# Performance work log

Measured on AMD Instinct MI355X. Metric: run time of the kernel, lower is better.

The kernel has to match this reference:

```python
import jax, jax.numpy as jnp
import numpy as np

B, T, F, H = 256, 4096, 16, 64

def setup_inputs() -> dict:
    key = jax.random.key(0)
    ks = jax.random.split(key, 16)
    rn = lambda k, s, sc=0.1: jax.random.normal(k, s, dtype=jnp.float32) * sc
    return {
        'x':    rn(ks[0], (B, T, F), 1.0),
        'Wi1':  rn(ks[1], (F, 3 * H)), 'bi1': jnp.zeros((3 * H,), jnp.float32),
        'Whr1': rn(ks[2], (H, H)), 'Whz1': rn(ks[3], (H, H)), 'Whn1': rn(ks[4], (H, H)),
        'bhn1': jnp.zeros((H,), jnp.float32),
        'Wi2':  rn(ks[5], (H, 3 * H)), 'bi2': jnp.zeros((3 * H,), jnp.float32),
        'Whr2': rn(ks[6], (H, H)), 'Whz2': rn(ks[7], (H, H)), 'Whn2': rn(ks[8], (H, H)),
        'bhn2': jnp.zeros((H,), jnp.float32),
        'Wp':   rn(ks[9], (F, H)), 'bp': jnp.zeros((H,), jnp.float32),
        'Wa':   rn(ks[10], (H, 1)), 'ba': jnp.zeros((1,), jnp.float32),
        'W1':   rn(ks[11], (H, 128)), 'b1': jnp.zeros((128,), jnp.float32),
        'W2':   rn(ks[12], (128, 64)), 'b2': jnp.zeros((64,), jnp.float32),
        'W3':   rn(ks[13], (64, 32)), 'b3': jnp.zeros((32,), jnp.float32),
        'W4':   rn(ks[14], (32, 2)), 'b4': jnp.zeros((2,), jnp.float32),
    }

def gru_layer(x, Wi, bi, Whr, Whz, Whn, bhn):
    # flax GRUCell math: r/z hidden kernels bias-free; n hidden kernel has bias.
    b, h = x.shape[0], Whr.shape[0]
    xi = jnp.einsum('btf,fk->btk', x, Wi) + bi  # precompute input projections (B,T,3H)
    def step(hprev, xt):
        ir, iz, inn = jnp.split(xt, 3, axis=-1)
        r = jax.nn.sigmoid(ir + hprev @ Whr)
        z = jax.nn.sigmoid(iz + hprev @ Whz)
        n = jnp.tanh(inn + r * (hprev @ Whn + bhn))
        hnew = (1.0 - z) * n + z * hprev
        return hnew, hnew
    h0 = jnp.zeros((b, h), x.dtype)
    _, ys = jax.lax.scan(step, h0, jnp.swapaxes(xi, 0, 1))  # (T,B,H)
    return jnp.swapaxes(ys, 0, 1)  # (B,T,H)

def reference(x, Wi1, bi1, Whr1, Whz1, Whn1, bhn1,
              Wi2, bi2, Whr2, Whz2, Whn2, bhn2,
              Wp, bp, Wa, ba, W1, b1, W2, b2, W3, b3, W4, b4):
    o1 = gru_layer(x, Wi1, bi1, Whr1, Whz1, Whn1, bhn1)
    x_proj = jnp.einsum('btf,fh->bth', x, Wp) + bp  # F != H -> project
    o1 = o1 + 0.5 * x_proj
    o2 = gru_layer(o1, Wi2, bi2, Whr2, Whz2, Whn2, bhn2) + 0.5 * o1
    scores = jnp.einsum('bth,ho->bto', o2, Wa) + ba  # (B,T,1)
    w = jax.nn.softmax(scores, axis=1)
    attended = jnp.sum(o2 * w, axis=1)  # (B,H)
    h1 = jax.nn.relu(attended @ W1 + b1)
    h2 = jax.nn.relu(h1 @ W2 + b2)
    h3 = jax.nn.relu(h2 @ W3 + b3)
    return h3 @ W4 + b4  # (B,2)
```

## Files before the change

kernel.cpp:

```cpp
#include <hip/hip_runtime.h>


#define B_ 256
#define T_ 4096
#define F_ 16
#define H_ 64
#define L2E 1.4426950408889634f

typedef float v2f __attribute__((ext_vector_type(2)));

__device__ __forceinline__ float rdlane(float v, int lane) {
    return __builtin_bit_cast(float, __builtin_amdgcn_readlane(__builtin_bit_cast(int, v), lane));
}
__device__ __forceinline__ float sigm(float x) {
    float e = __builtin_amdgcn_exp2f(-L2E * x);
    return __builtin_amdgcn_rcpf(1.0f + e);
}
__device__ __forceinline__ float tanh_(float x) {
    float e = __builtin_amdgcn_exp2f(2.0f * L2E * x);
    return 1.0f - 2.0f * __builtin_amdgcn_rcpf(1.0f + e);
}
__device__ __forceinline__ v2f fma2(v2f a, v2f b, v2f c) {
    return __builtin_elementwise_fma(a, b, c);
}

#define DPPADD(x, ctrl) \
    ((x) + __builtin_bit_cast(float, __builtin_amdgcn_update_dpp( \
        0, __builtin_bit_cast(int, (x)), (ctrl), 0xF, 0xF, true)))

__device__ __forceinline__ float qsum(float x) {
    float s = DPPADD(x, 0xB1);
    return DPPADD(s, 0x4E);
}
__device__ __forceinline__ float wred(float x) {
    x = DPPADD(x, 0x111);
    x = DPPADD(x, 0x112);
    x = DPPADD(x, 0x114);
    x = DPPADD(x, 0x118);
    x = DPPADD(x, 0x142);
    x = DPPADD(x, 0x143);
    return x;
}

__launch_bounds__(256, 1)
__global__ void solar_rnn(const float* __restrict__ x,
                          const float* __restrict__ Wi1, const float* __restrict__ bi1,
                          const float* __restrict__ Whr1, const float* __restrict__ Whz1,
                          const float* __restrict__ Whn1, const float* __restrict__ bhn1,
                          const float* __restrict__ Wi2, const float* __restrict__ bi2,
                          const float* __restrict__ Whr2, const float* __restrict__ Whz2,
                          const float* __restrict__ Whn2, const float* __restrict__ bhn2,
                          const float* __restrict__ Wp, const float* __restrict__ bp,
                          const float* __restrict__ Wa,
                          const float* __restrict__ W1, const float* __restrict__ b1,
                          const float* __restrict__ W2, const float* __restrict__ b2,
                          const float* __restrict__ W3, const float* __restrict__ b3,
                          const float* __restrict__ W4, const float* __restrict__ b4,
                          float* __restrict__ out)
{
    const int b   = blockIdx.x;
    const int tid = threadIdx.x;
    const int v   = tid >> 6;
    const int j   = tid & 63;
    const int oj  = 16 * v + (j >> 2);

    __shared__ __align__(16) float red[2][5][256][2];
    __shared__ float sp[2][64];
    __shared__ float sm_a[128];
    __shared__ float sm_b[128];

    const int wslot = (v + (j >> 3)) & 3;
    const int widx  = 4 * j + wslot;
    const int ridx  = 64 * v + j;

    v2f wr1p[8], wz1p[8], wn1p[8];
    v2f wr2p[8], wz2p[8], wn2p[8];
    v2f u2rp[8], u2zp[8], u2np[8];
    #pragma unroll
    for (int m = 0; m < 8; ++m) {
        const int r0 = 16 * v + 2 * m, r1 = r0 + 1;
        wr1p[m] = v2f{Whr1[r0 * H_ + j], Whr1[r1 * H_ + j]};
        wz1p[m] = v2f{Whz1[r0 * H_ + j], Whz1[r1 * H_ + j]};
        wn1p[m] = v2f{Whn1[r0 * H_ + j], Whn1[r1 * H_ + j]};
        wr2p[m] = v2f{Whr2[r0 * H_ + j], Whr2[r1 * H_ + j]};
        wz2p[m] = v2f{Whz2[r0 * H_ + j], Whz2[r1 * H_ + j]};
        wn2p[m] = v2f{Whn2[r0 * H_ + j], Whn2[r1 * H_ + j]};
        u2rp[m] = v2f{Wi2[r0 * 192 + j],       Wi2[r1 * 192 + j]};
        u2zp[m] = v2f{Wi2[r0 * 192 + 64 + j],  Wi2[r1 * 192 + 64 + j]};
        u2np[m] = v2f{Wi2[r0 * 192 + 128 + j], Wi2[r1 * 192 + 128 + j]};
    }
    float x2r[4], x2z[4], x2n[4];
    #pragma unroll
    for (int kk = 0; kk < 4; ++kk) {
        const int row = 4 * v + kk;
        float ar = 0.f, az = 0.f, an = 0.f;
        for (int m = 0; m < H_; ++m) {
            const float wp = Wp[row * H_ + m];
            ar = fmaf(wp, Wi2[m * 192 + j],       ar);
            az = fmaf(wp, Wi2[m * 192 + 64 + j],  az);
            an = fmaf(wp, Wi2[m * 192 + 128 + j], an);
        }
        x2r[kk] = 0.5f * ar; x2z[kk] = 0.5f * az; x2n[kk] = 0.5f * an;
    }
    v2f w1rp[2], w1zp[2], w1np[2], wpvp[2], x2rp[2], x2zp[2], x2np[2];
    #pragma unroll
    for (int m = 0; m < 2; ++m) {
        const int r0 = 4 * v + 2 * m, r1 = r0 + 1;
        w1rp[m] = v2f{Wi1[r0 * 192 + j],       Wi1[r1 * 192 + j]};
        w1zp[m] = v2f{Wi1[r0 * 192 + 64 + j],  Wi1[r1 * 192 + 64 + j]};
        w1np[m] = v2f{Wi1[r0 * 192 + 128 + j], Wi1[r1 * 192 + 128 + j]};
        wpvp[m] = v2f{Wp[r0 * H_ + j],         Wp[r1 * H_ + j]};
        x2rp[m] = v2f{x2r[2 * m], x2r[2 * m + 1]};
        x2zp[m] = v2f{x2z[2 * m], x2z[2 * m + 1]};
        x2np[m] = v2f{x2n[2 * m], x2n[2 * m + 1]};
    }
    float cbr = 0.f, cbz = 0.f, cbn = 0.f;
    for (int m = 0; m < H_; ++m) {
        const float bpm = bp[m];
        cbr = fmaf(bpm, Wi2[m * 192 + oj],       cbr);
        cbz = fmaf(bpm, Wi2[m * 192 + 64 + oj],  cbz);
        cbn = fmaf(bpm, Wi2[m * 192 + 128 + oj], cbn);
    }
    const float b1r = bi1[oj], b1z = bi1[64 + oj], b1n = bi1[128 + oj], bh1o = bhn1[oj];
    const float bb2r = bi2[oj]       + 0.5f * cbr;
    const float bb2z = bi2[64 + oj]  + 0.5f * cbz;
    const float bb2n = bi2[128 + oj] + 0.5f * cbn;
    const float bh2o = bhn2[oj];
    const float bpo  = bp[oj], wao = Wa[oj];

    float h1 = 0.f, h2 = 0.f, o1p = 0.f, o2a = 0.f;
    float am = -3.0e38f, al = 0.f, aa = 0.f;
    v2f sH1p[8], sH2p[8];
    #pragma unroll
    for (int m = 0; m < 8; ++m) { sH1p[m] = v2f{0.f, 0.f}; sH2p[m] = v2f{0.f, 0.f}; }

    const float* xb = x + (size_t)b * T_ * F_;
    float4 xq_cur  = *(const float4*)(xb + ((size_t)j * F_ + 4 * v));
    float4 xq_next = *(const float4*)(xb + ((size_t)(64 + j) * F_ + 4 * v));

    v2f cxp0, cxp1;

    {
        const float a0 = rdlane(xq_cur.x, 0), a1 = rdlane(xq_cur.y, 0),
                    a2 = rdlane(xq_cur.z, 0), a3 = rdlane(xq_cur.w, 0);
        const v2f ap0 = v2f{a0, a1}, ap1 = v2f{a2, a3};
        const v2f zz = v2f{0.f, 0.f};
        v2f arp = fma2(w1rp[0], ap0, fma2(w1rp[1], ap1, zz));
        v2f azp = fma2(w1zp[0], ap0, fma2(w1zp[1], ap1, zz));
        v2f anp = fma2(w1np[0], ap0, fma2(w1np[1], ap1, zz));
        v2f axp = fma2(wpvp[0], ap0, fma2(wpvp[1], ap1, zz));
        *(v2f*)&red[0][0][widx][0] = v2f{arp.x + arp.y, azp.x + azp.y};
        *(v2f*)&red[0][1][widx][0] = v2f{anp.x + anp.y, 0.f};
        *(v2f*)&red[0][2][widx][0] = v2f{axp.x + axp.y, 0.f};
        cxp0 = ap0; cxp1 = ap1;
    }
    __syncthreads();

    {
        const v2f q0 = *(const v2f*)&red[0][0][ridx][0];
        const v2f q1 = *(const v2f*)&red[0][1][ridx][0];
        const v2f q2 = *(const v2f*)&red[0][2][ridx][0];
        const float g0 = qsum(q0.x), g1 = qsum(q0.y);
        const float g2 = qsum(q1.x), g3 = qsum(q1.y);
        const float g4 = qsum(q2.x);
        const float r1 = sigm(g0 + b1r);
        const float z1 = sigm(g1 + b1z);
        const float n1 = tanh_((g2 + b1n) + r1 * (g3 + bh1o));
        h1 = n1 + z1 * (h1 - n1);
        o1p = h1 + 0.5f * (g4 + bpo);
        #pragma unroll
        for (int m = 0; m < 8; ++m)
            sH1p[m] = v2f{rdlane(h1, 8 * m), rdlane(h1, 8 * m + 4)};

        const float xn0 = rdlane(xq_cur.x, 1), xn1 = rdlane(xq_cur.y, 1),
                    xn2 = rdlane(xq_cur.z, 1), xn3 = rdlane(xq_cur.w, 1);
        const v2f xp0 = v2f{xn0, xn1}, xp1 = v2f{xn2, xn3};
        const v2f zz = v2f{0.f, 0.f};

        v2f Aar2 = fma2(x2rp[0], cxp0, fma2(x2rp[1], cxp1, zz));
        v2f Aaz2 = fma2(x2zp[0], cxp0, fma2(x2zp[1], cxp1, zz));
        v2f Aan2 = fma2(x2np[0], cxp0, fma2(x2np[1], cxp1, zz));
        #pragma unroll
        for (int m = 0; m < 8; ++m) {
            Aar2 = fma2(sH1p[m], u2rp[m], Aar2);
            Aaz2 = fma2(sH1p[m], u2zp[m], Aaz2);
            Aan2 = fma2(sH1p[m], u2np[m], Aan2);
        }
        v2f Aar1 = fma2(w1rp[0], xp0, fma2(w1rp[1], xp1, zz));
        v2f Aaz1 = fma2(w1zp[0], xp0, fma2(w1zp[1], xp1, zz));
        v2f Aan1 = fma2(w1np[0], xp0, fma2(w1np[1], xp1, zz));
        v2f Aax1 = fma2(wpvp[0], xp0, fma2(wpvp[1], xp1, zz));
        v2f Ahn1 = zz;
        #pragma unroll
        for (int m = 0; m < 8; ++m) {
            Aar1 = fma2(sH1p[m], wr1p[m], Aar1);
            Aaz1 = fma2(sH1p[m], wz1p[m], Aaz1);
            Ahn1 = fma2(sH1p[m], wn1p[m], Ahn1);
        }
        *(v2f*)&red[1][0][widx][0] = v2f{Aar1.x + Aar1.y, Aaz1.x + Aaz1.y};
        *(v2f*)&red[1][1][widx][0] = v2f{Aan1.x + Aan1.y, Ahn1.x + Ahn1.y};
        *(v2f*)&red[1][2][widx][0] = v2f{Aax1.x + Aax1.y, Aan2.x + Aan2.y};
        *(v2f*)&red[1][3][widx][0] = v2f{Aar2.x + Aar2.y, Aaz2.x + Aaz2.y};
        *(v2f*)&red[1][4][widx][0] = v2f{0.f, 0.f};
        cxp0 = xp0; cxp1 = xp1;
    }
    __syncthreads();

    #pragma unroll 1
    for (int t = 1; t < T_; ++t) {
        const int pb = t & 1, qb = pb ^ 1;
        const int u = t + 1;
        if ((u & 63) == 0) {
            xq_cur = xq_next;
            const int c = (u >> 6) + 1;
            if (c < T_ / 64)
                xq_next = *(const float4*)(xb + (size_t)(c * 64 + j) * F_ + 4 * v);
        }
        const int ul = u & 63;
        const v2f xp0 = v2f{rdlane(xq_cur.x, ul), rdlane(xq_cur.y, ul)};
        const v2f xp1 = v2f{rdlane(xq_cur.z, ul), rdlane(xq_cur.w, ul)};

        const v2f q0 = *(const v2f*)&red[pb][0][ridx][0];
        const v2f q1 = *(const v2f*)&red[pb][1][ridx][0];
        const v2f q2 = *(const v2f*)&red[pb][2][ridx][0];
        const v2f q3 = *(const v2f*)&red[pb][3][ridx][0];
        const v2f q4 = *(const v2f*)&red[pb][4][ridx][0];
        float gp = sp[pb][j & 3];

        const v2f zz = v2f{0.f, 0.f};
        v2f Aar1 = fma2(w1rp[0], xp0, fma2(w1rp[1], xp1, zz));
        v2f Aaz1 = fma2(w1zp[0], xp0, fma2(w1zp[1], xp1, zz));
        v2f Aan1 = fma2(w1np[0], xp0, fma2(w1np[1], xp1, zz));
        v2f Aax1 = fma2(wpvp[0], xp0, fma2(wpvp[1], xp1, zz));
        v2f Aar2 = fma2(x2rp[0], cxp0, fma2(x2rp[1], cxp1, zz));
        v2f Aaz2 = fma2(x2zp[0], cxp0, fma2(x2zp[1], cxp1, zz));
        v2f Aan2 = fma2(x2np[0], cxp0, fma2(x2np[1], cxp1, zz));
        v2f Ahn1 = zz, Ahn2 = zz;

        const float g0 = qsum(q0.x), g1 = qsum(q0.y);
        const float g2 = qsum(q1.x), g3 = qsum(q1.y);
        const float g4 = qsum(q2.x), g5 = qsum(q2.y);
        const float g6 = qsum(q3.x), g7 = qsum(q3.y);
        const float g8 = qsum(q4.x);
        gp = qsum(gp);

        if (t >= 2) {
            const float p  = 0.25f * gp;
            const float mn = fmaxf(am, p);
            const float ca = __builtin_amdgcn_exp2f((am - mn) * L2E);
            const float ce = __builtin_amdgcn_exp2f((p  - mn) * L2E);
            al = fmaf(al, ca, ce);
            aa = fmaf(aa, ca, ce * o2a);
            am = mn;
        }

        const float r2 = sigm(g6 + bb2r);
        const float z2 = sigm(g7 + bb2z);
        const float n2 = tanh_((g5 + bb2n) + r2 * (g8 + bh2o));
        h2 = n2 + z2 * (h2 - n2);
        const float o2 = h2 + 0.5f * o1p;
        float ps = wred(o2 * wao);
        if (j == 63) sp[qb][v] = ps;
        o2a = o2;
        #pragma unroll
        for (int m = 0; m < 8; ++m)
            sH2p[m] = v2f{rdlane(h2, 8 * m), rdlane(h2, 8 * m + 4)};

        const float r1 = sigm(g0 + b1r);
        const float z1 = sigm(g1 + b1z);
        const float n1 = tanh_((g2 + b1n) + r1 * (g3 + bh1o));
        h1 = n1 + z1 * (h1 - n1);
        o1p = h1 + 0.5f * (g4 + bpo);
        #pragma unroll
        for (int m = 0; m < 8; ++m)
            sH1p[m] = v2f{rdlane(h1, 8 * m), rdlane(h1, 8 * m + 4)};

        #pragma unroll
        for (int m = 0; m < 8; ++m) {
            Aar2 = fma2(sH2p[m], wr2p[m], Aar2);
            Aaz2 = fma2(sH2p[m], wz2p[m], Aaz2);
            Ahn2 = fma2(sH2p[m], wn2p[m], Ahn2);
        }
        #pragma unroll
        for (int m = 0; m < 8; ++m) {
            Aar2 = fma2(sH1p[m], u2rp[m], Aar2);
            Aaz2 = fma2(sH1p[m], u2zp[m], Aaz2);
            Aan2 = fma2(sH1p[m], u2np[m], Aan2);
        }
        #pragma unroll
        for (int m = 0; m < 8; ++m) {
            Aar1 = fma2(sH1p[m], wr1p[m], Aar1);
            Aaz1 = fma2(sH1p[m], wz1p[m], Aaz1);
            Ahn1 = fma2(sH1p[m], wn1p[m], Ahn1);
        }

        *(v2f*)&red[qb][0][widx][0] = v2f{Aar1.x + Aar1.y, Aaz1.x + Aaz1.y};
        *(v2f*)&red[qb][1][widx][0] = v2f{Aan1.x + Aan1.y, Ahn1.x + Ahn1.y};
        *(v2f*)&red[qb][2][widx][0] = v2f{Aax1.x + Aax1.y, Aan2.x + Aan2.y};
        *(v2f*)&red[qb][3][widx][0] = v2f{Aar2.x + Aar2.y, Aaz2.x + Aaz2.y};
        *(v2f*)&red[qb][4][widx][0] = v2f{Ahn2.x + Ahn2.y, 0.f};

        cxp0 = xp0; cxp1 = xp1;
        __syncthreads();
    }

    {
        const v2f q2 = *(const v2f*)&red[0][2][ridx][0];
        const v2f q3 = *(const v2f*)&red[0][3][ridx][0];
        const v2f q4 = *(const v2f*)&red[0][4][ridx][0];
        const float g5 = qsum(q2.y);
        const float g6 = qsum(q3.x), g7 = qsum(q3.y);
        const float g8 = qsum(q4.x);
        float gp = qsum(sp[0][j & 3]);
        {
            const float p  = 0.25f * gp;
            const float mn = fmaxf(am, p);
            const float ca = __builtin_amdgcn_exp2f((am - mn) * L2E);
            const float ce = __builtin_amdgcn_exp2f((p  - mn) * L2E);
            al = fmaf(al, ca, ce);
            aa = fmaf(aa, ca, ce * o2a);
            am = mn;
        }
        const float r2 = sigm(g6 + bb2r);
        const float z2 = sigm(g7 + bb2z);
        const float n2 = tanh_((g5 + bb2n) + r2 * (g8 + bh2o));
        h2 = n2 + z2 * (h2 - n2);
        const float o2 = h2 + 0.5f * o1p;
        float ps = wred(o2 * wao);
        if (j == 63) sp[1][v] = ps;
        __syncthreads();
        float gq = qsum(sp[1][j & 3]);
        {
            const float p  = 0.25f * gq;
            const float mn = fmaxf(am, p);
            const float ca = __builtin_amdgcn_exp2f((am - mn) * L2E);
            const float ce = __builtin_amdgcn_exp2f((p  - mn) * L2E);
            al = fmaf(al, ca, ce);
            aa = fmaf(aa, ca, ce * o2);
            am = mn;
        }
    }

    if ((j & 3) == 0) sm_a[oj] = aa / al;
    __syncthreads();

    float v1 = 0.f;
    if (tid < 128) {
        float a = b1[tid];
        for (int k = 0; k < 64; ++k) a = fmaf(sm_a[k], W1[k * 128 + tid], a);
        v1 = fmaxf(a, 0.f);
    }
    __syncthreads();
    if (tid < 128) sm_b[tid] = v1;
    __syncthreads();
    if (tid < 64) {
        float a = b2[tid];
        for (int k = 0; k < 128; ++k) a = fmaf(sm_b[k], W2[k * 64 + tid], a);
        sm_a[tid] = fmaxf(a, 0.f);
    }
    __syncthreads();
    if (tid < 32) {
        float a = b3[tid];
        for (int k = 0; k < 64; ++k) a = fmaf(sm_a[k], W3[k * 32 + tid], a);
        sm_b[tid] = fmaxf(a, 0.f);
    }
    __syncthreads();
    if (tid < 2) {
        float a = b4[tid];
        for (int k = 0; k < 32; ++k) a = fmaf(sm_b[k], W4[k * 2 + tid], a);
        out[b * 2 + tid] = a;
    }
}

extern "C" void kernel_launch(void* const* d_in, const int* in_sizes, int n_in,
                              void* d_out, int out_size, void* d_ws, size_t ws_size,
                              hipStream_t stream) {
    const float* x    = (const float*)d_in[0];
    const float* Wi1  = (const float*)d_in[1];
    const float* bi1  = (const float*)d_in[2];
    const float* Whr1 = (const float*)d_in[3];
    const float* Whz1 = (const float*)d_in[4];
    const float* Whn1 = (const float*)d_in[5];
    const float* bhn1 = (const float*)d_in[6];
    const float* Wi2  = (const float*)d_in[7];
    const float* bi2  = (const float*)d_in[8];
    const float* Whr2 = (const float*)d_in[9];
    const float* Whz2 = (const float*)d_in[10];
    const float* Whn2 = (const float*)d_in[11];
    const float* bhn2 = (const float*)d_in[12];
    const float* Wp   = (const float*)d_in[13];
    const float* bp   = (const float*)d_in[14];
    const float* Wa   = (const float*)d_in[15];
    const float* W1   = (const float*)d_in[17];
    const float* b1   = (const float*)d_in[18];
    const float* W2   = (const float*)d_in[19];
    const float* b2   = (const float*)d_in[20];
    const float* W3   = (const float*)d_in[21];
    const float* b3   = (const float*)d_in[22];
    const float* W4   = (const float*)d_in[23];
    const float* b4   = (const float*)d_in[24];

    solar_rnn<<<dim3(B_), dim3(256), 0, stream>>>(
        x, Wi1, bi1, Whr1, Whz1, Whn1, bhn1,
        Wi2, bi2, Whr2, Whz2, Whn2, bhn2,
        Wp, bp, Wa, W1, b1, W2, b2, W3, b3, W4, b4,
        (float*)d_out);
}
```

Before: 3.010 ms.

## Reorganize GRU recurrence so each quad owns an output column, exchanging hidden state via LDS

The recurrence is restructured so that each group of 4 lanes computes the full dot product for one output column, splitting the K dimension across the quad, and finishes with a quad DPP sum. Before, each wave handled a K-slice, hidden-state values were broadcast with readlane, and partial sums went through LDS. Now only the new h1/h2 vectors are written to double-buffered shared memory and read back as float4, which removes the 5-slot partial-sum exchange and the 16 readlanes per step. x is staged through a double-buffered LDS tile refilled every 16 steps, and the pipeline prologue is folded into the loop with a t==0 guard. The cost is more LDS reads per step and possible bank conflicts on the h vectors.

```diff
diff --git a/kernel.cpp b/kernel.cpp
--- a/kernel.cpp
+++ b/kernel.cpp
@@ -9,9 +9,6 @@
 
 typedef float v2f __attribute__((ext_vector_type(2)));
 
-__device__ __forceinline__ float rdlane(float v, int lane) {
-    return __builtin_bit_cast(float, __builtin_amdgcn_readlane(__builtin_bit_cast(int, v), lane));
-}
 __device__ __forceinline__ float sigm(float x) {
     float e = __builtin_amdgcn_exp2f(-L2E * x);
     return __builtin_amdgcn_rcpf(1.0f + e);
@@ -29,8 +26,8 @@
         0, __builtin_bit_cast(int, (x)), (ctrl), 0xF, 0xF, true)))
 
 __device__ __forceinline__ float qsum(float x) {
-    float s = DPPADD(x, 0xB1);
-    return DPPADD(s, 0x4E);
+    float t = DPPADD(x, 0xB1);
+    return DPPADD(t, 0x4E);
 }
 __device__ __forceinline__ float wred(float x) {
     x = DPPADD(x, 0x111);
@@ -62,54 +59,63 @@
     const int tid = threadIdx.x;
     const int v   = tid >> 6;
     const int j   = tid & 63;
-    const int oj  = 16 * v + (j >> 2);
-
-    __shared__ __align__(16) float red[2][5][256][2];
-    __shared__ float sp[2][64];
+    const int o   = j >> 2;
+    const int s   = j & 3;
+    const int col = 16 * v + o;
+
+    __shared__ __align__(16) float h1p[2][H_];
+    __shared__ __align__(16) float h2p[2][H_];
+    __shared__ __align__(16) float xbuf[2][256];
+    __shared__ float spl[2][4];
     __shared__ float sm_a[128];
     __shared__ float sm_b[128];
 
-    const int wslot = (v + (j >> 3)) & 3;
-    const int widx  = 4 * j + wslot;
-    const int ridx  = 64 * v + j;
+    int hoff[4];
+    #pragma unroll
+    for (int q = 0; q < 4; ++q) hoff[q] = 16 * s + 4 * ((q + s) & 3);
 
     v2f wr1p[8], wz1p[8], wn1p[8];
     v2f wr2p[8], wz2p[8], wn2p[8];
     v2f u2rp[8], u2zp[8], u2np[8];
     #pragma unroll
-    for (int m = 0; m < 8; ++m) {
-        const int r0 = 16 * v + 2 * m, r1 = r0 + 1;
-        wr1p[m] = v2f{Whr1[r0 * H_ + j], Whr1[r1 * H_ + j]};
-        wz1p[m] = v2f{Whz1[r0 * H_ + j], Whz1[r1 * H_ + j]};
-        wn1p[m] = v2f{Whn1[r0 * H_ + j], Whn1[r1 * H_ + j]};
-        wr2p[m] = v2f{Whr2[r0 * H_ + j], Whr2[r1 * H_ + j]};
-        wz2p[m] = v2f{Whz2[r0 * H_ + j], Whz2[r1 * H_ + j]};
-        wn2p[m] = v2f{Whn2[r0 * H_ + j], Whn2[r1 * H_ + j]};
-        u2rp[m] = v2f{Wi2[r0 * 192 + j],       Wi2[r1 * 192 + j]};
-        u2zp[m] = v2f{Wi2[r0 * 192 + 64 + j],  Wi2[r1 * 192 + 64 + j]};
-        u2np[m] = v2f{Wi2[r0 * 192 + 128 + j], Wi2[r1 * 192 + 128 + j]};
+    for (int q = 0; q < 4; ++q) {
+        const int rb = hoff[q];
+        #pragma unroll
+        for (int e = 0; e < 2; ++e) {
+            const int r0 = rb + 2 * e, r1 = r0 + 1;
+            const int m = 2 * q + e;
+            wr1p[m] = v2f{Whr1[r0 * H_ + col], Whr1[r1 * H_ + col]};
+            wz1p[m] = v2f{Whz1[r0 * H_ + col], Whz1[r1 * H_ + col]};
+            wn1p[m] = v2f{Whn1[r0 * H_ + col], Whn1[r1 * H_ + col]};
+            wr2p[m] = v2f{Whr2[r0 * H_ + col], Whr2[r1 * H_ + col]};
+            wz2p[m] = v2f{Whz2[r0 * H_ + col], Whz2[r1 * H_ + col]};
+            wn2p[m] = v2f{Whn2[r0 * H_ + col], Whn2[r1 * H_ + col]};
+            u2rp[m] = v2f{Wi2[r0 * 192 + col],       Wi2[r1 * 192 + col]};
+            u2zp[m] = v2f{Wi2[r0 * 192 + 64 + col],  Wi2[r1 * 192 + 64 + col]};
+            u2np[m] = v2f{Wi2[r0 * 192 + 128 + col], Wi2[r1 * 192 + 128 + col]};
+        }
     }
     float x2r[4], x2z[4], x2n[4];
     #pragma unroll
     for (int kk = 0; kk < 4; ++kk) {
-        const int row = 4 * v + kk;
+        const int row = 4 * s + kk;
         float ar = 0.f, az = 0.f, an = 0.f;
         for (int m = 0; m < H_; ++m) {
             const float wp = Wp[row * H_ + m];
-            ar = fmaf(wp, Wi2[m * 192 + j],       ar);
-            az = fmaf(wp, Wi2[m * 192 + 64 + j],  az);
-            an = fmaf(wp, Wi2[m * 192 + 128 + j], an);
+            ar = fmaf(wp, Wi2[m * 192 + col],       ar);
+            az = fmaf(wp, Wi2[m * 192 + 64 + col],  az);
+            an = fmaf(wp, Wi2[m * 192 + 128 + col], an);
         }
         x2r[kk] = 0.5f * ar; x2z[kk] = 0.5f * az; x2n[kk] = 0.5f * an;
     }
     v2f w1rp[2], w1zp[2], w1np[2], wpvp[2], x2rp[2], x2zp[2], x2np[2];
     #pragma unroll
     for (int m = 0; m < 2; ++m) {
-        const int r0 = 4 * v + 2 * m, r1 = r0 + 1;
-        w1rp[m] = v2f{Wi1[r0 * 192 + j],       Wi1[r1 * 192 + j]};
-        w1zp[m] = v2f{Wi1[r0 * 192 + 64 + j],  Wi1[r1 * 192 + 64 + j]};
-        w1np[m] = v2f{Wi1[r0 * 192 + 128 + j], Wi1[r1 * 192 + 128 + j]};
-        wpvp[m] = v2f{Wp[r0 * H_ + j],         Wp[r1 * H_ + j]};
+        const int r0 = 4 * s + 2 * m, r1 = r0 + 1;
+        w1rp[m] = v2f{Wi1[r0 * 192 + col],       Wi1[r1 * 192 + col]};
+        w1zp[m] = v2f{Wi1[r0 * 192 + 64 + col],  Wi1[r1 * 192 + 64 + col]};
+        w1np[m] = v2f{Wi1[r0 * 192 + 128 + col], Wi1[r1 * 192 + 128 + col]};
+        wpvp[m] = v2f{Wp[r0 * H_ + col],         Wp[r1 * H_ + col]};
         x2rp[m] = v2f{x2r[2 * m], x2r[2 * m + 1]};
         x2zp[m] = v2f{x2z[2 * m], x2z[2 * m + 1]};
         x2np[m] = v2f{x2n[2 * m], x2n[2 * m + 1]};
@@ -117,131 +123,82 @@
     float cbr = 0.f, cbz = 0.f, cbn = 0.f;
     for (int m = 0; m < H_; ++m) {
         const float bpm = bp[m];
-        cbr = fmaf(bpm, Wi2[m * 192 + oj],       cbr);
-        cbz = fmaf(bpm, Wi2[m * 192 + 64 + oj],  cbz);
-        cbn = fmaf(bpm, Wi2[m * 192 + 128 + oj], cbn);
-    }
-    const float b1r = bi1[oj], b1z = bi1[64 + oj], b1n = bi1[128 + oj], bh1o = bhn1[oj];
-    const float bb2r = bi2[oj]       + 0.5f * cbr;
-    const float bb2z = bi2[64 + oj]  + 0.5f * cbz;
-    const float bb2n = bi2[128 + oj] + 0.5f * cbn;
-    const float bh2o = bhn2[oj];
-    const float bpo  = bp[oj], wao = Wa[oj];
+        cbr = fmaf(bpm, Wi2[m * 192 + col],       cbr);
+        cbz = fmaf(bpm, Wi2[m * 192 + 64 + col],  cbz);
+        cbn = fmaf(bpm, Wi2[m * 192 + 128 + col], cbn);
+    }
+    const float b1r = bi1[col], b1z = bi1[64 + col], b1n = bi1[128 + col], bh1o = bhn1[col];
+    const float bb2r = bi2[col]       + 0.5f * cbr;
+    const float bb2z = bi2[64 + col]  + 0.5f * cbz;
+    const float bb2n = bi2[128 + col] + 0.5f * cbn;
+    const float bh2o = bhn2[col];
+    const float bpo  = bp[col], wao = Wa[col];
+
+    if (tid < 64) { h1p[0][j] = 0.f; h1p[1][j] = 0.f; h2p[0][j] = 0.f; h2p[1][j] = 0.f; }
+    if (tid < 8)  spl[tid >> 2][tid & 3] = 0.f;
+    const float* xb = x + (size_t)b * T_ * F_;
+    float4 xnext;
+    if (tid < 64) {
+        const float4* gx = (const float4*)xb;
+        ((float4*)xbuf[0])[j] = gx[j];
+        xnext = gx[64 + j];
+    }
+    __syncthreads();
 
     float h1 = 0.f, h2 = 0.f, o1p = 0.f, o2a = 0.f;
     float am = -3.0e38f, al = 0.f, aa = 0.f;
-    v2f sH1p[8], sH2p[8];
-    #pragma unroll
-    for (int m = 0; m < 8; ++m) { sH1p[m] = v2f{0.f, 0.f}; sH2p[m] = v2f{0.f, 0.f}; }
-
-    const float* xb = x + (size_t)b * T_ * F_;
-    float4 xq_cur  = *(const float4*)(xb + ((size_t)j * F_ + 4 * v));
-    float4 xq_next = *(const float4*)(xb + ((size_t)(64 + j) * F_ + 4 * v));
-
-    v2f cxp0, cxp1;
-
-    {
-        const float a0 = rdlane(xq_cur.x, 0), a1 = rdlane(xq_cur.y, 0),
-                    a2 = rdlane(xq_cur.z, 0), a3 = rdlane(xq_cur.w, 0);
-        const v2f ap0 = v2f{a0, a1}, ap1 = v2f{a2, a3};
+    v2f xprev0 = v2f{0.f, 0.f}, xprev1 = v2f{0.f, 0.f};
+
+    #pragma unroll 1
+    for (int t = 0; t < T_; ++t) {
+        const int tb = t & 1;
+
+        const float4 xt4 = ((const float4*)xbuf[(t >> 4) & 1])[(t & 15) * 4 + s];
+        const float* h1r = h1p[tb ^ 1];
+        const float* h2r = h2p[tb];
+        v2f hv1[8], hv2[8];
+        #pragma unroll
+        for (int q = 0; q < 4; ++q) {
+            const float4 a = *(const float4*)&h1r[hoff[q]];
+            const float4 c = *(const float4*)&h2r[hoff[q]];
+            hv1[2 * q]     = v2f{a.x, a.y};
+            hv1[2 * q + 1] = v2f{a.z, a.w};
+            hv2[2 * q]     = v2f{c.x, c.y};
+            hv2[2 * q + 1] = v2f{c.z, c.w};
+        }
+        float gp = spl[tb][s];
+
         const v2f zz = v2f{0.f, 0.f};
-        v2f arp = fma2(w1rp[0], ap0, fma2(w1rp[1], ap1, zz));
-        v2f azp = fma2(w1zp[0], ap0, fma2(w1zp[1], ap1, zz));
-        v2f anp = fma2(w1np[0], ap0, fma2(w1np[1], ap1, zz));
-        v2f axp = fma2(wpvp[0], ap0, fma2(wpvp[1], ap1, zz));
-        *(v2f*)&red[0][0][widx][0] = v2f{arp.x + arp.y, azp.x + azp.y};
-        *(v2f*)&red[0][1][widx][0] = v2f{anp.x + anp.y, 0.f};
-        *(v2f*)&red[0][2][widx][0] = v2f{axp.x + axp.y, 0.f};
-        cxp0 = ap0; cxp1 = ap1;
-    }
-    __syncthreads();
-
-    {
-        const v2f q0 = *(const v2f*)&red[0][0][ridx][0];
-        const v2f q1 = *(const v2f*)&red[0][1][ridx][0];
-        const v2f q2 = *(const v2f*)&red[0][2][ridx][0];
-        const float g0 = qsum(q0.x), g1 = qsum(q0.y);
-        const float g2 = qsum(q1.x), g3 = qsum(q1.y);
-        const float g4 = qsum(q2.x);
-        const float r1 = sigm(g0 + b1r);
-        const float z1 = sigm(g1 + b1z);
-        const float n1 = tanh_((g2 + b1n) + r1 * (g3 + bh1o));
-        h1 = n1 + z1 * (h1 - n1);
-        o1p = h1 + 0.5f * (g4 + bpo);
-        #pragma unroll
-        for (int m = 0; m < 8; ++m)
-            sH1p[m] = v2f{rdlane(h1, 8 * m), rdlane(h1, 8 * m + 4)};
-
-        const float xn0 = rdlane(xq_cur.x, 1), xn1 = rdlane(xq_cur.y, 1),
-                    xn2 = rdlane(xq_cur.z, 1), xn3 = rdlane(xq_cur.w, 1);
-        const v2f xp0 = v2f{xn0, xn1}, xp1 = v2f{xn2, xn3};
-        const v2f zz = v2f{0.f, 0.f};
-
-        v2f Aar2 = fma2(x2rp[0], cxp0, fma2(x2rp[1], cxp1, zz));
-        v2f Aaz2 = fma2(x2zp[0], cxp0, fma2(x2zp[1], cxp1, zz));
-        v2f Aan2 = fma2(x2np[0], cxp0, fma2(x2np[1], cxp1, zz));
+        v2f Aar2 = fma2(x2rp[0], xprev0, fma2(x2rp[1], xprev1, zz));
+        v2f Aaz2 = fma2(x2zp[0], xprev0, fma2(x2zp[1], xprev1, zz));
+        v2f Aan2 = fma2(x2np[0], xprev0, fma2(x2np[1], xprev1, zz));
+        const v2f xt0 = v2f{xt4.x, xt4.y}, xt1 = v2f{xt4.z, xt4.w};
+        v2f Aar1 = fma2(w1rp[0], xt0, fma2(w1rp[1], xt1, zz));
+        v2f Aaz1 = fma2(w1zp[0], xt0, fma2(w1zp[1], xt1, zz));
+        v2f Aan1 = fma2(w1np[0], xt0, fma2(w1np[1], xt1, zz));
+        v2f Aax1 = fma2(wpvp[0], xt0, fma2(wpvp[1], xt1, zz));
+        v2f Ahn1 = zz, Ahn2 = zz;
         #pragma unroll
         for (int m = 0; m < 8; ++m) {
-            Aar2 = fma2(sH1p[m], u2rp[m], Aar2);
-            Aaz2 = fma2(sH1p[m], u2zp[m], Aaz2);
-            Aan2 = fma2(sH1p[m], u2np[m], Aan2);
-        }
-        v2f Aar1 = fma2(w1rp[0], xp0, fma2(w1rp[1], xp1, zz));
-        v2f Aaz1 = fma2(w1zp[0], xp0, fma2(w1zp[1], xp1, zz));
-        v2f Aan1 = fma2(w1np[0], xp0, fma2(w1np[1], xp1, zz));
-        v2f Aax1 = fma2(wpvp[0], xp0, fma2(wpvp[1], xp1, zz));
-        v2f Ahn1 = zz;
-        #pragma unroll
-        for (int m = 0; m < 8; ++m) {
-            Aar1 = fma2(sH1p[m], wr1p[m], Aar1);
-            Aaz1 = fma2(sH1p[m], wz1p[m], Aaz1);
-            Ahn1 = fma2(sH1p[m], wn1p[m], Ahn1);
-        }
-        *(v2f*)&red[1][0][widx][0] = v2f{Aar1.x + Aar1.y, Aaz1.x + Aaz1.y};
-        *(v2f*)&red[1][1][widx][0] = v2f{Aan1.x + Aan1.y, Ahn1.x + Ahn1.y};
-        *(v2f*)&red[1][2][widx][0] = v2f{Aax1.x + Aax1.y, Aan2.x + Aan2.y};
-        *(v2f*)&red[1][3][widx][0] = v2f{Aar2.x + Aar2.y, Aaz2.x + Aaz2.y};
-        *(v2f*)&red[1][4][widx][0] = v2f{0.f, 0.f};
-        cxp0 = xp0; cxp1 = xp1;
-    }
-    __syncthreads();
-
-    #pragma unroll 1
-    for (int t = 1; t < T_; ++t) {
-        const int pb = t & 1, qb = pb ^ 1;
-        const int u = t + 1;
-        if ((u & 63) == 0) {
-            xq_cur = xq_next;
-            const int c = (u >> 6) + 1;
-            if (c < T_ / 64)
-                xq_next = *(const float4*)(xb + (size_t)(c * 64 + j) * F_ + 4 * v);
-        }
-        const int ul = u & 63;
-        const v2f xp0 = v2f{rdlane(xq_cur.x, ul), rdlane(xq_cur.y, ul)};
-        const v2f xp1 = v2f{rdlane(xq_cur.z, ul), rdlane(xq_cur.w, ul)};
-
-        const v2f q0 = *(const v2f*)&red[pb][0][ridx][0];
-        const v2f q1 = *(const v2f*)&red[pb][1][ridx][0];
-        const v2f q2 = *(const v2f*)&red[pb][2][ridx][0];
-        const v2f q3 = *(const v2f*)&red[pb][3][ridx][0];
-        const v2f q4 = *(const v2f*)&red[pb][4][ridx][0];
-        float gp = sp[pb][j & 3];
-
-        const v2f zz = v2f{0.f, 0.f};
-        v2f Aar1 = fma2(w1rp[0], xp0, fma2(w1rp[1], xp1, zz));
-        v2f Aaz1 = fma2(w1zp[0], xp0, fma2(w1zp[1], xp1, zz));
-        v2f Aan1 = fma2(w1np[0], xp0, fma2(w1np[1], xp1, zz));
-        v2f Aax1 = fma2(wpvp[0], xp0, fma2(wpvp[1], xp1, zz));
-        v2f Aar2 = fma2(x2rp[0], cxp0, fma2(x2rp[1], cxp1, zz));
-        v2f Aaz2 = fma2(x2zp[0], cxp0, fma2(x2zp[1], cxp1, zz));
-        v2f Aan2 = fma2(x2np[0], cxp0, fma2(x2np[1], cxp1, zz));
-        v2f Ahn1 = zz, Ahn2 = zz;
-
-        const float g0 = qsum(q0.x), g1 = qsum(q0.y);
-        const float g2 = qsum(q1.x), g3 = qsum(q1.y);
-        const float g4 = qsum(q2.x), g5 = qsum(q2.y);
-        const float g6 = qsum(q3.x), g7 = qsum(q3.y);
-        const float g8 = qsum(q4.x);
+            Aar1 = fma2(hv1[m], wr1p[m], Aar1);
+            Aaz1 = fma2(hv1[m], wz1p[m], Aaz1);
+            Ahn1 = fma2(hv1[m], wn1p[m], Ahn1);
+            Aar2 = fma2(hv1[m], u2rp[m], Aar2);
+            Aaz2 = fma2(hv1[m], u2zp[m], Aaz2);
+            Aan2 = fma2(hv1[m], u2np[m], Aan2);
+            Aar2 = fma2(hv2[m], wr2p[m], Aar2);
+            Aaz2 = fma2(hv2[m], wz2p[m], Aaz2);
+            Ahn2 = fma2(hv2[m], wn2p[m], Ahn2);
+        }
+        const float g0 = qsum(Aar1.x + Aar1.y);
+        const float g1 = qsum(Aaz1.x + Aaz1.y);
+        const float g2 = qsum(Aan1.x + Aan1.y);
+        const float g3 = qsum(Ahn1.x + Ahn1.y);
+        const float g4 = qsum(Aax1.x + Aax1.y);
+        const float g5 = qsum(Aan2.x + Aan2.y);
+        const float g6 = qsum(Aar2.x + Aar2.y);
+        const float g7 = qsum(Aaz2.x + Aaz2.y);
+        const float g8 = qsum(Ahn2.x + Ahn2.y);
         gp = qsum(gp);
 
         if (t >= 2) {
@@ -258,60 +215,63 @@
         const float z2 = sigm(g7 + bb2z);
         const float n2 = tanh_((g5 + bb2n) + r2 * (g8 + bh2o));
         h2 = n2 + z2 * (h2 - n2);
+        h2 = (t == 0) ? 0.f : h2;
         const float o2 = h2 + 0.5f * o1p;
         float ps = wred(o2 * wao);
-        if (j == 63) sp[qb][v] = ps;
+        if (j == 63) spl[tb ^ 1][v] = ps;
+        if (s == 0) h2p[tb ^ 1][col] = h2;
         o2a = o2;
-        #pragma unroll
-        for (int m = 0; m < 8; ++m)
-            sH2p[m] = v2f{rdlane(h2, 8 * m), rdlane(h2, 8 * m + 4)};
 
         const float r1 = sigm(g0 + b1r);
         const float z1 = sigm(g1 + b1z);
         const float n1 = tanh_((g2 + b1n) + r1 * (g3 + bh1o));
         h1 = n1 + z1 * (h1 - n1);
         o1p = h1 + 0.5f * (g4 + bpo);
-        #pragma unroll
-        for (int m = 0; m < 8; ++m)
-            sH1p[m] = v2f{rdlane(h1, 8 * m), rdlane(h1, 8 * m + 4)};
-
+        if (s == 0) h1p[tb][col] = h1;
+
+        if ((t & 15) == 8 && tid < 64) {
+            const int c = t >> 4;
+            if (c + 1 < T_ / 16) {
+                ((float4*)xbuf[(c + 1) & 1])[j] = xnext;
+                if (c + 2 < T_ / 16) xnext = ((const float4*)xb)[(c + 2) * 64 + j];
+            }
+        }
+        xprev0 = xt0; xprev1 = xt1;
+        __syncthreads();
+    }
+
+    {
+        const float* h1r = h1p[1];
+        const float* h2r = h2p[0];
+        v2f hv1[8], hv2[8];
+        #pragma unroll
+        for (int q = 0; q < 4; ++q) {
+            const float4 a = *(const float4*)&h1r[hoff[q]];
+            const float4 c = *(const float4*)&h2r[hoff[q]];
+            hv1[2 * q]     = v2f{a.x, a.y};
+            hv1[2 * q + 1] = v2f{a.z, a.w};
+            hv2[2 * q]     = v2f{c.x, c.y};
+            hv2[2 * q + 1] = v2f{c.z, c.w};
+        }
+        const v2f zz = v2f{0.f, 0.f};
+        v2f Aar2 = fma2(x2rp[0], xprev0, fma2(x2rp[1], xprev1, zz));
+        v2f Aaz2 = fma2(x2zp[0], xprev0, fma2(x2zp[1], xprev1, zz));
+        v2f Aan2 = fma2(x2np[0], xprev0, fma2(x2np[1], xprev1, zz));
+        v2f Ahn2 = zz;
         #pragma unroll
         for (int m = 0; m < 8; ++m) {
-            Aar2 = fma2(sH2p[m], wr2p[m], Aar2);
-            Aaz2 = fma2(sH2p[m], wz2p[m], Aaz2);
-            Ahn2 = fma2(sH2p[m], wn2p[m], Ahn2);
-        }
-        #pragma unroll
-        for (int m = 0; m < 8; ++m) {
-            Aar2 = fma2(sH1p[m], u2rp[m], Aar2);
-            Aaz2 = fma2(sH1p[m], u2zp[m], Aaz2);
-            Aan2 = fma2(sH1p[m], u2np[m], Aan2);
-        }
-        #pragma unroll
-        for (int m = 0; m < 8; ++m) {
-            Aar1 = fma2(sH1p[m], wr1p[m], Aar1);
-            Aaz1 = fma2(sH1p[m], wz1p[m], Aaz1);
-            Ahn1 = fma2(sH1p[m], wn1p[m], Ahn1);
-        }
-
-        *(v2f*)&red[qb][0][widx][0] = v2f{Aar1.x + Aar1.y, Aaz1.x + Aaz1.y};
-        *(v2f*)&red[qb][1][widx][0] = v2f{Aan1.x + Aan1.y, Ahn1.x + Ahn1.y};
-        *(v2f*)&red[qb][2][widx][0] = v2f{Aax1.x + Aax1.y, Aan2.x + Aan2.y};
-        *(v2f*)&red[qb][3][widx][0] = v2f{Aar2.x + Aar2.y, Aaz2.x + Aaz2.y};
-        *(v2f*)&red[qb][4][widx][0] = v2f{Ahn2.x + Ahn2.y, 0.f};
-
-        cxp0 = xp0; cxp1 = xp1;
-        __syncthreads();
-    }
-
-    {
-        const v2f q2 = *(const v2f*)&red[0][2][ridx][0];
-        const v2f q3 = *(const v2f*)&red[0][3][ridx][0];
-        const v2f q4 = *(const v2f*)&red[0][4][ridx][0];
-        const float g5 = qsum(q2.y);
-        const float g6 = qsum(q3.x), g7 = qsum(q3.y);
-        const float g8 = qsum(q4.x);
-        float gp = qsum(sp[0][j & 3]);
+            Aar2 = fma2(hv1[m], u2rp[m], Aar2);
+            Aaz2 = fma2(hv1[m], u2zp[m], Aaz2);
+            Aan2 = fma2(hv1[m], u2np[m], Aan2);
+            Aar2 = fma2(hv2[m], wr2p[m], Aar2);
+            Aaz2 = fma2(hv2[m], wz2p[m], Aaz2);
+            Ahn2 = fma2(hv2[m], wn2p[m], Ahn2);
+        }
+        const float g5 = qsum(Aan2.x + Aan2.y);
+        const float g6 = qsum(Aar2.x + Aar2.y);
+        const float g7 = qsum(Aaz2.x + Aaz2.y);
+        const float g8 = qsum(Ahn2.x + Ahn2.y);
+        float gp = qsum(spl[0][s]);
         {
             const float p  = 0.25f * gp;
             const float mn = fmaxf(am, p);
@@ -327,9 +287,9 @@
         h2 = n2 + z2 * (h2 - n2);
         const float o2 = h2 + 0.5f * o1p;
         float ps = wred(o2 * wao);
-        if (j == 63) sp[1][v] = ps;
+        if (j == 63) spl[1][v] = ps;
         __syncthreads();
-        float gq = qsum(sp[1][j & 3]);
+        float gq = qsum(spl[1][s]);
         {
             const float p  = 0.25f * gq;
             const float mn = fmaxf(am, p);
@@ -341,7 +301,7 @@
         }
     }
 
-    if ((j & 3) == 0) sm_a[oj] = aa / al;
+    if (s == 0) sm_a[col] = aa / al;
     __syncthreads();
 
     float v1 = 0.f;
```

Result: faster. 2.619 ms (-13.0%).
